# Performance work log

Hardware: AMD Instinct MI355X
Metric: run time of the kernel (lower is better)

Reference implementation:

```python
import jax, jax.numpy as jnp
import numpy as np

D_MODEL = 256
N_HEAD = 8
HEAD_DIM = D_MODEL // N_HEAD
N_TOTAL = 24576
B, T = 64, 512


def setup_inputs() -> dict:
    key = jax.random.key(0)
    ks = jax.random.split(key, 12)
    s = 1.0 / np.sqrt(D_MODEL)
    return {
        "x": jax.random.normal(ks[0], (N_TOTAL, D_MODEL), jnp.float32),
        "Wq": jax.random.uniform(ks[1], (D_MODEL, D_MODEL), jnp.float32, -s, s),
        "bq": jax.random.uniform(ks[2], (D_MODEL,), jnp.float32, -s, s),
        "Wk": jax.random.uniform(ks[3], (D_MODEL, D_MODEL), jnp.float32, -s, s),
        "bk": jax.random.uniform(ks[4], (D_MODEL,), jnp.float32, -s, s),
        "Wv": jax.random.uniform(ks[5], (D_MODEL, D_MODEL), jnp.float32, -s, s),
        "bv": jax.random.uniform(ks[6], (D_MODEL,), jnp.float32, -s, s),
        "Wp": jax.random.uniform(ks[7], (D_MODEL, D_MODEL), jnp.float32, -s, s),
        "bp": jax.random.uniform(ks[8], (D_MODEL,), jnp.float32, -s, s),
        "padpack_index": jax.random.randint(ks[9], (B, T), 0, N_TOTAL, jnp.int64 if jax.config.jax_enable_x64 else jnp.int32),
        "padpack_batch": jax.random.randint(ks[10], (B, T), 0, B, jnp.int32),
        "padpack_inverse_index": jax.random.randint(ks[11], (N_TOTAL,), 0, B * T, jnp.int64 if jax.config.jax_enable_x64 else jnp.int32),
    }


def reference(x, Wq, bq, Wk, bk, Wv, bv, Wp, bp, padpack_index, padpack_batch, padpack_inverse_index):
    # gather ragged tokens into packed [B, T, C]
    xp = x[padpack_index]
    # mask: True where packed slots share the same segment id (matches
    # original masked_fill(batch_i == batch_j, -1e9))
    mask = padpack_batch[:, :, None] == padpack_batch[:, None, :]  # [B,T,T]
    # QKV projections (torch Linear: x @ W.T + b), split heads
    def heads(w, b):
        h = xp @ w.T + b
        return h.reshape(B, T, N_HEAD, HEAD_DIM).transpose(0, 2, 1, 3)  # [B,H,T,D]
    q, k, v = heads(Wq, bq), heads(Wk, bk), heads(Wv, bv)
    att = jnp.einsum("bhtd,bhsd->bhts", q, k) * (1.0 / np.sqrt(HEAD_DIM))
    att = jnp.where(mask[:, None], jnp.float32(-1e9), att)
    att = jax.nn.softmax(att, axis=-1)
    y = jnp.einsum("bhts,bhsd->bhtd", att, v)  # [B,H,T,D]
    y = y.transpose(0, 2, 1, 3).reshape(B, T, D_MODEL)
    y = y @ Wp.T + bp
    # scatter back to ragged layout
    return y.reshape(B * T, D_MODEL)[padpack_inverse_index]
```

## Files before the change

### kernel.cpp

```cpp
#include <hip/hip_runtime.h>


typedef __attribute__((ext_vector_type(8))) short short8;
typedef __attribute__((ext_vector_type(4))) float f32x4;

#define N_TOTAL 24576
#define B_ 64
#define T_ 512
#define DM 256
#define NH 8
#define HD 32
#define F3 768

#define QSCALE 0.25503463f
#define VSP 530

__device__ __forceinline__ unsigned short f2bf(float f) {
  unsigned int u = __float_as_uint(f);
  u += 0x7fffu + ((u >> 16) & 1u);
  return (unsigned short)(u >> 16);
}

__device__ __forceinline__ void gl_lds16(const void* g, void* l) {
  __builtin_amdgcn_global_load_lds(
      (const __attribute__((address_space(1))) unsigned int*)g,
      (__attribute__((address_space(3))) unsigned int*)l, 16, 0, 0);
}

__global__ __launch_bounds__(256) void pack_kernel(
    const float* __restrict__ Wq, const float* __restrict__ Wk,
    const float* __restrict__ Wv, const float* __restrict__ Wp,
    const float* __restrict__ bq, const float* __restrict__ bk,
    const float* __restrict__ bv,
    short* __restrict__ WCAT, short* __restrict__ WPb,
    float* __restrict__ BCAT) {
  int gid = blockIdx.x * 256 + threadIdx.x;
  if (gid < 768)
    BCAT[gid] = (gid < 256) ? bq[gid] : (gid < 512 ? bk[gid - 256] : bv[gid - 512]);
  const float* src;
  short* dst;
  if (gid < 24576) {
    int f = gid >> 5, seg = gid & 31;
    const float* W = (f < 256) ? Wq : ((f < 512) ? Wk : Wv);
    src = W + (size_t)(f & 255) * DM + seg * 8;
    dst = WCAT + (size_t)gid * 8;
  } else {
    int u = gid - 24576;
    src = Wp + (size_t)u * 8;
    dst = WPb + (size_t)u * 8;
  }
  const float4* s4 = (const float4*)src;
  float4 a = s4[0], b = s4[1];
  short8 o;
  o[0] = (short)f2bf(a.x); o[1] = (short)f2bf(a.y);
  o[2] = (short)f2bf(a.z); o[3] = (short)f2bf(a.w);
  o[4] = (short)f2bf(b.x); o[5] = (short)f2bf(b.y);
  o[6] = (short)f2bf(b.z); o[7] = (short)f2bf(b.w);
  *(short8*)dst = o;
}

__global__ __launch_bounds__(256) void qkv_gemm(
    const float* __restrict__ x, const int* __restrict__ idx,
    const short* __restrict__ WCAT, const float* __restrict__ BCAT,
    unsigned short* __restrict__ QKVp) {
  __shared__ __align__(16) char Asm[8 * 4096];
  __shared__ __align__(16) char Bsm[3 * 8192];
  int tid = threadIdx.x;
  int lane = tid & 63, w = tid >> 6;
  int i = lane & 15, q = lane >> 4;
  int m0 = blockIdx.x * 64;
  int wn = w * 32;
  int csa = q ^ ((i >> 1) & 3);

  int row = tid >> 2, c = tid & 3;
  int cs0 = c ^ ((row >> 1) & 3);
  int brow1 = 64 + row;
  int cs1 = c ^ ((brow1 >> 1) & 3);
  const float* ax = x + (size_t)idx[m0 + row] * DM;

  auto issueB = [&](int g, int s) {
    int p = g >> 3, k = g & 7;
    gl_lds16(WCAT + (size_t)(p * 128 + row) * DM + k * 32 + cs0 * 8,
             Bsm + s * 8192 + tid * 16);
    gl_lds16(WCAT + (size_t)(p * 128 + brow1) * DM + k * 32 + cs1 * 8,
             Bsm + s * 8192 + (256 + tid) * 16);
  };

  issueB(0, 0);
  issueB(1, 1);
#pragma unroll
  for (int k = 0; k < 8; k++) {
    float4 lo = *(const float4*)(ax + k * 32 + cs0 * 8);
    float4 hi = *(const float4*)(ax + k * 32 + cs0 * 8 + 4);
    short8 o;
    o[0] = (short)f2bf(lo.x); o[1] = (short)f2bf(lo.y);
    o[2] = (short)f2bf(lo.z); o[3] = (short)f2bf(lo.w);
    o[4] = (short)f2bf(hi.x); o[5] = (short)f2bf(hi.y);
    o[6] = (short)f2bf(hi.z); o[7] = (short)f2bf(hi.w);
    *(short8*)(Asm + k * 4096 + tid * 16) = o;
  }
  asm volatile("s_waitcnt vmcnt(2) lgkmcnt(0)\ns_barrier" ::: "memory");

  f32x4 zf = {0.f, 0.f, 0.f, 0.f};
  f32x4 acc[4][2];
#pragma unroll
  for (int mt = 0; mt < 4; mt++) {
    acc[mt][0] = zf;
    acc[mt][1] = zf;
  }

#pragma unroll 1
  for (int p = 0; p < 6; p++) {
#pragma unroll
    for (int k = 0; k < 8; k++) {
      int g = p * 8 + k;
      if (g > 0) {
        if (g == 47)
          asm volatile("s_waitcnt vmcnt(0) lgkmcnt(0)\ns_barrier" ::: "memory");
        else
          asm volatile("s_waitcnt vmcnt(2) lgkmcnt(0)\ns_barrier" ::: "memory");
      }
      const short* Asb = (const short*)(Asm + k * 4096);
      const short* Bsb = (const short*)(Bsm + (g % 3) * 8192);
      short8 a[4], bfr[2];
#pragma unroll
      for (int mt = 0; mt < 4; mt++)
        a[mt] = *(const short8*)&Asb[(mt * 16 + i) * 32 + csa * 8];
#pragma unroll
      for (int nt = 0; nt < 2; nt++)
        bfr[nt] = *(const short8*)&Bsb[(wn + nt * 16 + i) * 32 + csa * 8];
      if (g + 2 < 48) issueB(g + 2, (g + 2) % 3);
#pragma unroll
      for (int mt = 0; mt < 4; mt++) {
        acc[mt][0] = __builtin_amdgcn_mfma_f32_16x16x32_bf16(a[mt], bfr[0], acc[mt][0], 0, 0, 0);
        acc[mt][1] = __builtin_amdgcn_mfma_f32_16x16x32_bf16(a[mt], bfr[1], acc[mt][1], 0, 0, 0);
      }
    }
    float scale = (p < 2) ? QSCALE : 1.0f;
#pragma unroll
    for (int nt = 0; nt < 2; nt++) {
      int f = p * 128 + wn + nt * 16 + i;
      float bias = BCAT[f];
#pragma unroll
      for (int mt = 0; mt < 4; mt++) {
#pragma unroll
        for (int r = 0; r < 4; r++) {
          int token = m0 + mt * 16 + q * 4 + r;
          QKVp[(size_t)token * F3 + f] = f2bf((acc[mt][nt][r] + bias) * scale);
        }
        acc[mt][nt] = zf;
      }
    }
  }
}

__global__ __launch_bounds__(512, 4) void attn_kernel(
    const unsigned short* __restrict__ QKVp, const int* __restrict__ batch,
    unsigned short* __restrict__ Y) {
  __shared__ __align__(16) short Vl[HD * VSP];
  __shared__ int sbat[T_];
  int tid = threadIdx.x, w = tid >> 6, lane = tid & 63;
  int i = lane & 15, q = lane >> 4;
  int bx = blockIdx.x;
  int h = bx >> 6, b = bx & 63;
  int t0 = w * 64;
  const unsigned short* Tok = QKVp + (size_t)b * T_ * F3;

  sbat[tid] = batch[b * T_ + tid];

  {
    int seg = tid & 3, sb = tid >> 2;
#pragma unroll
    for (int l = 0; l < 4; l++) {
      int s = sb + l * 128;
      short8 v = *(const short8*)&Tok[(size_t)s * F3 + 512 + h * HD + seg * 8];
#pragma unroll
      for (int j = 0; j < 8; j++) Vl[(seg * 8 + j) * VSP + s] = v[j];
    }
  }
  __syncthreads();

  short8 qf[4];
  int btm[4];
#pragma unroll
  for (int mt = 0; mt < 4; mt++)
    qf[mt] = *(const short8*)&Tok[(size_t)(t0 + mt * 16 + i) * F3 + h * HD + q * 8];
#pragma unroll
  for (int mt = 0; mt < 4; mt++) btm[mt] = sbat[t0 + mt * 16 + i];

  unsigned short ob = (i == 0) ? (unsigned short)0x3F80 : (unsigned short)0;
  short8 ones = {(short)ob, (short)ob, (short)ob, (short)ob,
                 (short)ob, (short)ob, (short)ob, (short)ob};

  f32x4 zf = {0.f, 0.f, 0.f, 0.f};
  f32x4 o[4][2], lacc[4];
#pragma unroll
  for (int mt = 0; mt < 4; mt++) {
    o[mt][0] = zf; o[mt][1] = zf; lacc[mt] = zf;
  }

  const unsigned short* Kb = Tok + 256 + h * HD + q * 8;
  short8 k0f = *(const short8*)&Kb[(size_t)(i)*F3];
  short8 k1f = *(const short8*)&Kb[(size_t)(16 + i) * F3];

  for (int s0 = 0; s0 < T_; s0 += 32) {
    short8 ck0 = k0f, ck1 = k1f;
    if (s0 + 32 < T_) {
      k0f = *(const short8*)&Kb[(size_t)(s0 + 32 + i) * F3];
      k1f = *(const short8*)&Kb[(size_t)(s0 + 48 + i) * F3];
    }
    int4 bs0 = *(const int4*)&sbat[s0 + q * 4];
    int4 bs1 = *(const int4*)&sbat[s0 + 16 + q * 4];
    short8 v0f = *(const short8*)&Vl[i * VSP + s0 + q * 8];
    short8 v1f = *(const short8*)&Vl[(16 + i) * VSP + s0 + q * 8];
#pragma unroll
    for (int mt = 0; mt < 4; mt++) {
      f32x4 st0 = __builtin_amdgcn_mfma_f32_16x16x32_bf16(ck0, qf[mt], zf, 0, 0, 0);
      f32x4 st1 = __builtin_amdgcn_mfma_f32_16x16x32_bf16(ck1, qf[mt], zf, 0, 0, 0);
      int bm = btm[mt];
      float e00 = __builtin_amdgcn_exp2f((bs0.x == bm) ? -1e9f : st0[0]);
      float e01 = __builtin_amdgcn_exp2f((bs0.y == bm) ? -1e9f : st0[1]);
      float e02 = __builtin_amdgcn_exp2f((bs0.z == bm) ? -1e9f : st0[2]);
      float e03 = __builtin_amdgcn_exp2f((bs0.w == bm) ? -1e9f : st0[3]);
      float e10 = __builtin_amdgcn_exp2f((bs1.x == bm) ? -1e9f : st1[0]);
      float e11 = __builtin_amdgcn_exp2f((bs1.y == bm) ? -1e9f : st1[1]);
      float e12 = __builtin_amdgcn_exp2f((bs1.z == bm) ? -1e9f : st1[2]);
      float e13 = __builtin_amdgcn_exp2f((bs1.w == bm) ? -1e9f : st1[3]);
      unsigned A0 = __builtin_amdgcn_perm(__float_as_uint(e01), __float_as_uint(e00), 0x07060302u);
      unsigned A1 = __builtin_amdgcn_perm(__float_as_uint(e03), __float_as_uint(e02), 0x07060302u);
      unsigned B0 = __builtin_amdgcn_perm(__float_as_uint(e11), __float_as_uint(e10), 0x07060302u);
      unsigned B1 = __builtin_amdgcn_perm(__float_as_uint(e13), __float_as_uint(e12), 0x07060302u);
      asm volatile(
          "s_nop 1\n\t"
          "v_permlane32_swap_b32 %0, %2\n\t"
          "v_permlane32_swap_b32 %1, %3\n\t"
          "s_nop 1\n\t"
          "v_permlane16_swap_b32 %0, %2\n\t"
          "v_permlane16_swap_b32 %1, %3\n\t"
          "s_nop 1"
          : "+v"(A0), "+v"(A1), "+v"(B0), "+v"(B1));
      union {
        unsigned u[4];
        short8 s;
      } cv;
      cv.u[0] = A0;
      cv.u[1] = A1;
      cv.u[2] = B0;
      cv.u[3] = B1;
      short8 pa = cv.s;
      o[mt][0] = __builtin_amdgcn_mfma_f32_16x16x32_bf16(pa, v0f, o[mt][0], 0, 0, 0);
      o[mt][1] = __builtin_amdgcn_mfma_f32_16x16x32_bf16(pa, v1f, o[mt][1], 0, 0, 0);
      lacc[mt] = __builtin_amdgcn_mfma_f32_16x16x32_bf16(pa, ones, lacc[mt], 0, 0, 0);
    }
  }

#pragma unroll
  for (int mt = 0; mt < 4; mt++) {
#pragma unroll
    for (int r = 0; r < 4; r++) {
      float lv = __shfl(lacc[mt][r], lane & 48, 64);
      float inv = __builtin_amdgcn_rcpf(lv);
      size_t yb = ((size_t)b * T_ + t0 + mt * 16 + q * 4 + r) * DM + h * HD;
      Y[yb + i] = f2bf(o[mt][0][r] * inv);
      Y[yb + 16 + i] = f2bf(o[mt][1][r] * inv);
    }
  }
}

__global__ __launch_bounds__(256) void out_gemm(
    const short* __restrict__ Y, const short* __restrict__ WPb,
    const float* __restrict__ bp, const int* __restrict__ inv,
    float* __restrict__ out) {
  __shared__ __align__(16) char smem[3 * 16384];
  int tid = threadIdx.x;
  int lane = tid & 63, w = tid >> 6;
  int i = lane & 15, q = lane >> 4;
  int m0 = blockIdx.x * 128, n0 = blockIdx.y * 128;
  int wm = (w & 1) * 64, wn = (w >> 1) * 64;
  int csa = q ^ ((i >> 1) & 3);

  int iv0 = inv[m0 + (tid >> 2)];
  int iv1 = inv[m0 + 64 + (tid >> 2)];

  f32x4 zf = {0.f, 0.f, 0.f, 0.f};
  f32x4 acc[4][4];
#pragma unroll
  for (int mt = 0; mt < 4; mt++)
#pragma unroll
    for (int nt = 0; nt < 4; nt++) acc[mt][nt] = zf;

  auto stage = [&](int k, int s) {
#pragma unroll
    for (int p = 0; p < 2; p++) {
      int U = p * 256 + tid;
      int row = U >> 2, c = U & 3;
      int cs = c ^ ((row >> 1) & 3);
      int iv = p ? iv1 : iv0;
      gl_lds16(Y + (size_t)iv * DM + k * 32 + cs * 8, smem + s * 16384 + U * 16);
      gl_lds16(WPb + (size_t)(n0 + row) * DM + k * 32 + cs * 8,
               smem + s * 16384 + 8192 + U * 16);
    }
  };

  stage(0, 0);
  stage(1, 1);
#pragma unroll
  for (int k = 0; k < 8; k++) {
    if (k == 7)
      asm volatile("s_waitcnt vmcnt(0) lgkmcnt(0)\ns_barrier" ::: "memory");
    else
      asm volatile("s_waitcnt vmcnt(4) lgkmcnt(0)\ns_barrier" ::: "memory");
    const short* Asb = (const short*)(smem + (k % 3) * 16384);
    const short* Bsb = Asb + 4096;
    short8 a[4], bfr[4];
#pragma unroll
    for (int mt = 0; mt < 4; mt++)
      a[mt] = *(const short8*)&Asb[(wm + mt * 16 + i) * 32 + csa * 8];
#pragma unroll
    for (int nt = 0; nt < 4; nt++)
      bfr[nt] = *(const short8*)&Bsb[(wn + nt * 16 + i) * 32 + csa * 8];
    if (k < 6) stage(k + 2, (k + 2) % 3);
#pragma unroll
    for (int mt = 0; mt < 4; mt++)
#pragma unroll
      for (int nt = 0; nt < 4; nt++)
        acc[mt][nt] = __builtin_amdgcn_mfma_f32_16x16x32_bf16(a[mt], bfr[nt], acc[mt][nt], 0, 0, 0);
  }

#pragma unroll
  for (int nt = 0; nt < 4; nt++) {
    int f = n0 + wn + nt * 16 + i;
    float bias = bp[f];
#pragma unroll
    for (int mt = 0; mt < 4; mt++) {
#pragma unroll
      for (int r = 0; r < 4; r++) {
        int row = m0 + wm + mt * 16 + q * 4 + r;
        out[(size_t)row * DM + f] = acc[mt][nt][r] + bias;
      }
    }
  }
}

extern "C" void kernel_launch(void* const* d_in, const int* in_sizes, int n_in,
                              void* d_out, int out_size, void* d_ws, size_t ws_size,
                              hipStream_t stream) {
  const float* x = (const float*)d_in[0];
  const float* Wq = (const float*)d_in[1];
  const float* bq = (const float*)d_in[2];
  const float* Wk = (const float*)d_in[3];
  const float* bk = (const float*)d_in[4];
  const float* Wv = (const float*)d_in[5];
  const float* bv = (const float*)d_in[6];
  const float* Wp = (const float*)d_in[7];
  const float* bp = (const float*)d_in[8];
  const int* idx = (const int*)d_in[9];
  const int* batch = (const int*)d_in[10];
  const int* inv = (const int*)d_in[11];
  float* out = (float*)d_out;

  char* ws = (char*)d_ws;
  short* WCAT = (short*)(ws + 0);
  short* WPb = (short*)(ws + 524288);
  float* BCAT = (float*)(ws + 1048576);
  unsigned short* QKVp = (unsigned short*)(ws + 2097152);
  unsigned short* Yb = (unsigned short*)(ws + 52428800);

  pack_kernel<<<128, 256, 0, stream>>>(Wq, Wk, Wv, Wp, bq, bk, bv,
                                       WCAT, WPb, BCAT);
  qkv_gemm<<<512, 256, 0, stream>>>(x, idx, WCAT, BCAT, QKVp);
  attn_kernel<<<512, 512, 0, stream>>>(QKVp, batch, Yb);
  out_gemm<<<dim3(192, 2), 256, 0, stream>>>((const short*)Yb, WPb, bp, inv, out);
}
```

Before: 163.9 us.

## Fold weight bf16 packing into QKV GEMM and attention kernels, drop pack kernel

Removes the separate pack_kernel launch. The QKV GEMM now loads fp32 weight tiles into registers, converts them to bf16 and writes them to LDS itself, replacing the direct global-to-LDS async copies with a register-staged double-buffer pipeline. Bias is read straight from bq/bk/bv, and the first 32 attention blocks convert Wp to bf16 for the later out_gemm. This saves one launch and one weight round-trip through memory. In exchange, all 512 GEMM blocks redundantly convert the weights and spend more VGPRs and VALU work, and loads now go through registers instead of async LDS copies.

```diff
diff --git a/kernel.cpp b/kernel.cpp
--- a/kernel.cpp
+++ b/kernel.cpp
@@ -2,6 +2,7 @@
 
 
 typedef __attribute__((ext_vector_type(8))) short short8;
+typedef __attribute__((ext_vector_type(4))) short short4_t;
 typedef __attribute__((ext_vector_type(4))) float f32x4;
 
 #define N_TOTAL 24576
@@ -27,41 +28,11 @@
       (__attribute__((address_space(3))) unsigned int*)l, 16, 0, 0);
 }
 
-__global__ __launch_bounds__(256) void pack_kernel(
-    const float* __restrict__ Wq, const float* __restrict__ Wk,
-    const float* __restrict__ Wv, const float* __restrict__ Wp,
-    const float* __restrict__ bq, const float* __restrict__ bk,
-    const float* __restrict__ bv,
-    short* __restrict__ WCAT, short* __restrict__ WPb,
-    float* __restrict__ BCAT) {
-  int gid = blockIdx.x * 256 + threadIdx.x;
-  if (gid < 768)
-    BCAT[gid] = (gid < 256) ? bq[gid] : (gid < 512 ? bk[gid - 256] : bv[gid - 512]);
-  const float* src;
-  short* dst;
-  if (gid < 24576) {
-    int f = gid >> 5, seg = gid & 31;
-    const float* W = (f < 256) ? Wq : ((f < 512) ? Wk : Wv);
-    src = W + (size_t)(f & 255) * DM + seg * 8;
-    dst = WCAT + (size_t)gid * 8;
-  } else {
-    int u = gid - 24576;
-    src = Wp + (size_t)u * 8;
-    dst = WPb + (size_t)u * 8;
-  }
-  const float4* s4 = (const float4*)src;
-  float4 a = s4[0], b = s4[1];
-  short8 o;
-  o[0] = (short)f2bf(a.x); o[1] = (short)f2bf(a.y);
-  o[2] = (short)f2bf(a.z); o[3] = (short)f2bf(a.w);
-  o[4] = (short)f2bf(b.x); o[5] = (short)f2bf(b.y);
-  o[6] = (short)f2bf(b.z); o[7] = (short)f2bf(b.w);
-  *(short8*)dst = o;
-}
-
 __global__ __launch_bounds__(256) void qkv_gemm(
     const float* __restrict__ x, const int* __restrict__ idx,
-    const short* __restrict__ WCAT, const float* __restrict__ BCAT,
+    const float* __restrict__ Wq, const float* __restrict__ Wk,
+    const float* __restrict__ Wv, const float* __restrict__ bq,
+    const float* __restrict__ bk, const float* __restrict__ bv,
     unsigned short* __restrict__ QKVp) {
   __shared__ __align__(16) char Asm[8 * 4096];
   __shared__ __align__(16) char Bsm[3 * 8192];
@@ -78,16 +49,41 @@
   int cs1 = c ^ ((brow1 >> 1) & 3);
   const float* ax = x + (size_t)idx[m0 + row] * DM;
 
-  auto issueB = [&](int g, int s) {
-    int p = g >> 3, k = g & 7;
-    gl_lds16(WCAT + (size_t)(p * 128 + row) * DM + k * 32 + cs0 * 8,
-             Bsm + s * 8192 + tid * 16);
-    gl_lds16(WCAT + (size_t)(p * 128 + brow1) * DM + k * 32 + cs1 * 8,
-             Bsm + s * 8192 + (256 + tid) * 16);
+  auto wrow = [&](int f) -> const float* {
+    const float* Wb = (f < 256) ? Wq : ((f < 512) ? Wk : Wv);
+    return Wb + (size_t)(f & 255) * DM;
   };
 
-  issueB(0, 0);
-  issueB(1, 1);
+  float4 fb[2][2][2];
+
+  auto issueBloads = [&](int g, int par) {
+    int p2 = g >> 3, k2 = g & 7;
+    const float* s0 = wrow(p2 * 128 + row) + k2 * 32 + cs0 * 8;
+    const float* s1 = wrow(p2 * 128 + brow1) + k2 * 32 + cs1 * 8;
+    fb[par][0][0] = *(const float4*)(s0);
+    fb[par][0][1] = *(const float4*)(s0 + 4);
+    fb[par][1][0] = *(const float4*)(s1);
+    fb[par][1][1] = *(const float4*)(s1 + 4);
+  };
+  auto writeB = [&](int g, int par) {
+    char* dst = Bsm + (g % 3) * 8192;
+    short8 o0, o1;
+    float4 l0 = fb[par][0][0], h0 = fb[par][0][1];
+    float4 l1 = fb[par][1][0], h1 = fb[par][1][1];
+    o0[0] = (short)f2bf(l0.x); o0[1] = (short)f2bf(l0.y);
+    o0[2] = (short)f2bf(l0.z); o0[3] = (short)f2bf(l0.w);
+    o0[4] = (short)f2bf(h0.x); o0[5] = (short)f2bf(h0.y);
+    o0[6] = (short)f2bf(h0.z); o0[7] = (short)f2bf(h0.w);
+    o1[0] = (short)f2bf(l1.x); o1[1] = (short)f2bf(l1.y);
+    o1[2] = (short)f2bf(l1.z); o1[3] = (short)f2bf(l1.w);
+    o1[4] = (short)f2bf(h1.x); o1[5] = (short)f2bf(h1.y);
+    o1[6] = (short)f2bf(h1.z); o1[7] = (short)f2bf(h1.w);
+    *(short8*)(dst + tid * 16) = o0;
+    *(short8*)(dst + (256 + tid) * 16) = o1;
+  };
+
+  issueBloads(0, 0);
+  issueBloads(1, 1);
 #pragma unroll
   for (int k = 0; k < 8; k++) {
     float4 lo = *(const float4*)(ax + k * 32 + cs0 * 8);
@@ -99,7 +95,7 @@
     o[6] = (short)f2bf(hi.z); o[7] = (short)f2bf(hi.w);
     *(short8*)(Asm + k * 4096 + tid * 16) = o;
   }
-  asm volatile("s_waitcnt vmcnt(2) lgkmcnt(0)\ns_barrier" ::: "memory");
+  writeB(0, 0);
 
   f32x4 zf = {0.f, 0.f, 0.f, 0.f};
   f32x4 acc[4][2];
@@ -114,12 +110,7 @@
 #pragma unroll
     for (int k = 0; k < 8; k++) {
       int g = p * 8 + k;
-      if (g > 0) {
-        if (g == 47)
-          asm volatile("s_waitcnt vmcnt(0) lgkmcnt(0)\ns_barrier" ::: "memory");
-        else
-          asm volatile("s_waitcnt vmcnt(2) lgkmcnt(0)\ns_barrier" ::: "memory");
-      }
+      asm volatile("s_waitcnt lgkmcnt(0)\ns_barrier" ::: "memory");
       const short* Asb = (const short*)(Asm + k * 4096);
       const short* Bsb = (const short*)(Bsm + (g % 3) * 8192);
       short8 a[4], bfr[2];
@@ -129,18 +120,21 @@
 #pragma unroll
       for (int nt = 0; nt < 2; nt++)
         bfr[nt] = *(const short8*)&Bsb[(wn + nt * 16 + i) * 32 + csa * 8];
-      if (g + 2 < 48) issueB(g + 2, (g + 2) % 3);
+      if (g + 2 < 48) issueBloads(g + 2, k & 1);
 #pragma unroll
       for (int mt = 0; mt < 4; mt++) {
         acc[mt][0] = __builtin_amdgcn_mfma_f32_16x16x32_bf16(a[mt], bfr[0], acc[mt][0], 0, 0, 0);
         acc[mt][1] = __builtin_amdgcn_mfma_f32_16x16x32_bf16(a[mt], bfr[1], acc[mt][1], 0, 0, 0);
       }
+      if (g + 1 < 48) writeB(g + 1, (k + 1) & 1);
     }
     float scale = (p < 2) ? QSCALE : 1.0f;
+    const float* bb = (p < 2) ? bq : ((p < 4) ? bk : bv);
+    int boff = (p < 2) ? 0 : ((p < 4) ? 256 : 512);
 #pragma unroll
     for (int nt = 0; nt < 2; nt++) {
       int f = p * 128 + wn + nt * 16 + i;
-      float bias = BCAT[f];
+      float bias = bb[f - boff];
 #pragma unroll
       for (int mt = 0; mt < 4; mt++) {
 #pragma unroll
@@ -156,6 +150,7 @@
 
 __global__ __launch_bounds__(512, 4) void attn_kernel(
     const unsigned short* __restrict__ QKVp, const int* __restrict__ batch,
+    const float* __restrict__ Wp, short* __restrict__ WPb,
     unsigned short* __restrict__ Y) {
   __shared__ __align__(16) short Vl[HD * VSP];
   __shared__ int sbat[T_];
@@ -167,6 +162,15 @@
   const unsigned short* Tok = QKVp + (size_t)b * T_ * F3;
 
   sbat[tid] = batch[b * T_ + tid];
+
+  if (bx < 32) {
+    int u = bx * 512 + tid;
+    float4 v = ((const float4*)Wp)[u];
+    short4_t o;
+    o[0] = (short)f2bf(v.x); o[1] = (short)f2bf(v.y);
+    o[2] = (short)f2bf(v.z); o[3] = (short)f2bf(v.w);
+    *(short4_t*)(WPb + (size_t)u * 4) = o;
+  }
 
   {
     int seg = tid & 3, sb = tid >> 2;
@@ -360,15 +364,11 @@
   float* out = (float*)d_out;
 
   char* ws = (char*)d_ws;
-  short* WCAT = (short*)(ws + 0);
   short* WPb = (short*)(ws + 524288);
-  float* BCAT = (float*)(ws + 1048576);
   unsigned short* QKVp = (unsigned short*)(ws + 2097152);
   unsigned short* Yb = (unsigned short*)(ws + 52428800);
 
-  pack_kernel<<<128, 256, 0, stream>>>(Wq, Wk, Wv, Wp, bq, bk, bv,
-                                       WCAT, WPb, BCAT);
-  qkv_gemm<<<512, 256, 0, stream>>>(x, idx, WCAT, BCAT, QKVp);
-  attn_kernel<<<512, 512, 0, stream>>>(QKVp, batch, Yb);
+  qkv_gemm<<<512, 256, 0, stream>>>(x, idx, Wq, Wk, Wv, bq, bk, bv, QKVp);
+  attn_kernel<<<512, 512, 0, stream>>>(QKVp, batch, Wp, WPb, Yb);
   out_gemm<<<dim3(192, 2), 256, 0, stream>>>((const short*)Yb, WPb, bp, inv, out);
 }
```

New measurement: 168.6 us. 1.03x slower.
